# Optimization experiments

Measured on AMD Instinct MI355X. Metric: run time of the kernel, lower is better.

The kernel has to match this reference:

```python
import jax, jax.numpy as jnp
import numpy as np

N_NODES = 50000
N_EDGES = 800000
IN_FEATS = 64
OUT_FEATS = 64
EDGE_DIM = 8


def setup_inputs() -> dict:
    key = jax.random.key(0)
    k1, k2, k3, k4, k5 = jax.random.split(key, 5)
    node_feat = jax.random.normal(k1, (N_NODES, IN_FEATS), dtype=jnp.float32)
    edge_feat = jax.random.normal(k2, (N_EDGES, EDGE_DIM), dtype=jnp.float32)
    W = jax.random.normal(k3, (OUT_FEATS, IN_FEATS), dtype=jnp.float32) * (1.0 / np.sqrt(IN_FEATS))
    b = jnp.zeros((OUT_FEATS,), dtype=jnp.float32)
    src = jax.random.randint(k4, (N_EDGES,), 0, N_NODES, dtype=jnp.int64 if jax.config.jax_enable_x64 else jnp.int32)
    dst = jax.random.randint(k5, (N_EDGES,), 0, N_NODES, dtype=jnp.int64 if jax.config.jax_enable_x64 else jnp.int32)
    return {"node_feat": node_feat, "edge_feat": edge_feat, "W": W, "b": b,
            "src": src, "dst": dst}


def reference(node_feat, edge_feat, W, b, src, dst):
    # EfConv forward with aggregate='sum', node_feat.shape[1] == in_feats.
    n_nodes = node_feat.shape[0]
    edge_dim = edge_feat.shape[1]
    h_src = node_feat[src]  # [E, in_feats] gather once, reused for every slice
    aggs = []
    for k in range(edge_dim):  # small fixed loop over edge feature slices
        m = h_src * edge_feat[:, k:k + 1]                      # u_mul_e: [E, in_feats]
        aggs.append(jax.ops.segment_sum(m, dst, num_segments=n_nodes))
    agg = jnp.stack(aggs, axis=1)                              # [N, edge_dim, in_feats]
    # per-slice shared linear, then concat along feature dim
    out = jnp.einsum('nki,oi->nko', agg, W) + b                # [N, edge_dim, out_feats]
    return out.reshape(n_nodes, edge_dim * W.shape[0])         # [N, edge_dim*out_feats]
```

## Files before the change

kernel.cpp:

```cpp
#include <hip/hip_runtime.h>


#define FEATS 64
#define EDGE_DIM 8

typedef _Float16 half8 __attribute__((ext_vector_type(8)));

__global__ void __launch_bounds__(256) transform_kernel(
    const float* __restrict__ nf, const float* __restrict__ W,
    _Float16* __restrict__ t, int* __restrict__ deg, int n_nodes)
{
    __shared__ float sWt[FEATS * 65];
    __shared__ float srow[4][FEATS];
    const int tid = threadIdx.x;

    int gid = blockIdx.x * 256 + tid;
    if (gid < n_nodes) deg[gid] = 0;

    #pragma unroll
    for (int base = 0; base < FEATS * FEATS; base += 256) {
        int idx = base + tid;
        int o = idx >> 6;
        int i = idx & 63;
        sWt[i * 65 + o] = W[idx];
    }

    const int r = tid >> 6;
    const int o = tid & 63;
    const int node = blockIdx.x * 4 + r;
    if (node < n_nodes) srow[r][o] = nf[(long)node * FEATS + o];
    __syncthreads();

    if (node >= n_nodes) return;
    float sum = 0.f;
    #pragma unroll
    for (int i = 0; i < FEATS; i++)
        sum += srow[r][i] * sWt[i * 65 + o];
    t[(long)node * FEATS + o] = (_Float16)sum;
}

__global__ void __launch_bounds__(256) hist_kernel(
    const int* __restrict__ dst, int* __restrict__ deg,
    int* __restrict__ rank, int n_edges)
{
    int i4 = (blockIdx.x * 256 + threadIdx.x) * 4;
    if (i4 + 3 < n_edges) {
        int4 d = *(const int4*)(dst + i4);
        int4 r;
        r.x = atomicAdd(&deg[d.x], 1);
        r.y = atomicAdd(&deg[d.y], 1);
        r.z = atomicAdd(&deg[d.z], 1);
        r.w = atomicAdd(&deg[d.w], 1);
        *(int4*)(rank + i4) = r;
    } else {
        for (int e = i4; e < n_edges; ++e)
            rank[e] = atomicAdd(&deg[dst[e]], 1);
    }
}

__global__ void __launch_bounds__(256) partials_kernel(
    const int* __restrict__ deg, int* __restrict__ partials, int n)
{
    __shared__ int s[256];
    int i = blockIdx.x * 256 + threadIdx.x;
    s[threadIdx.x] = (i < n) ? deg[i] : 0;
    __syncthreads();
    for (int off = 128; off > 0; off >>= 1) {
        if (threadIdx.x < off) s[threadIdx.x] += s[threadIdx.x + off];
        __syncthreads();
    }
    if (threadIdx.x == 0) partials[blockIdx.x] = s[0];
}

__global__ void __launch_bounds__(256) scan_partials_kernel(
    const int* __restrict__ partials, int* __restrict__ pscan, int nb)
{
    __shared__ int s[256];
    int tid = threadIdx.x;
    s[tid] = (tid < nb) ? partials[tid] : 0;
    for (int off = 1; off < 256; off <<= 1) {
        __syncthreads();
        int x = (tid >= off) ? s[tid - off] : 0;
        __syncthreads();
        s[tid] += x;
    }
    __syncthreads();
    pscan[tid] = (tid == 0) ? 0 : s[tid - 1];
}

__global__ void __launch_bounds__(256) scan_addback_kernel(
    const int* __restrict__ deg, const int* __restrict__ pscan,
    int* __restrict__ offsets, int n, int n_edges)
{
    __shared__ int s[256];
    int tid = threadIdx.x;
    int i = blockIdx.x * 256 + tid;
    int v = (i < n) ? deg[i] : 0;
    s[tid] = v;
    for (int off = 1; off < 256; off <<= 1) {
        __syncthreads();
        int x = (tid >= off) ? s[tid - off] : 0;
        __syncthreads();
        s[tid] += x;
    }
    __syncthreads();
    if (i < n)
        offsets[i] = pscan[blockIdx.x] + s[tid] - v;
    if (blockIdx.x == 0 && tid == 0) offsets[n] = n_edges;
}

__global__ void __launch_bounds__(256) permute_ef_kernel(
    const int* __restrict__ src, const int* __restrict__ dst,
    const int* __restrict__ rank, const int* __restrict__ offsets,
    const float* __restrict__ ef,
    int* __restrict__ srcs, half8* __restrict__ efs, int n_edges)
{
    int i4 = (blockIdx.x * 256 + threadIdx.x) * 4;
    if (i4 + 3 < n_edges) {
        int4 s = *(const int4*)(src + i4);
        int4 d = *(const int4*)(dst + i4);
        int4 r = *(const int4*)(rank + i4);
        const float4* q = (const float4*)(ef + (long)i4 * EDGE_DIM);
        int p0 = offsets[d.x] + r.x;
        int p1 = offsets[d.y] + r.y;
        int p2 = offsets[d.z] + r.z;
        int p3 = offsets[d.w] + r.w;
        #pragma unroll
        for (int u = 0; u < 4; u++) {
            float4 a = q[2 * u], c = q[2 * u + 1];
            half8 h;
            h[0] = (_Float16)a.x; h[1] = (_Float16)a.y;
            h[2] = (_Float16)a.z; h[3] = (_Float16)a.w;
            h[4] = (_Float16)c.x; h[5] = (_Float16)c.y;
            h[6] = (_Float16)c.z; h[7] = (_Float16)c.w;
            int p = (u == 0) ? p0 : (u == 1) ? p1 : (u == 2) ? p2 : p3;
            efs[p] = h;
        }
        srcs[p0] = s.x; srcs[p1] = s.y; srcs[p2] = s.z; srcs[p3] = s.w;
    } else {
        for (int e = i4; e < n_edges; ++e) {
            int p = offsets[dst[e]] + rank[e];
            srcs[p] = src[e];
            const float* q = ef + (long)e * EDGE_DIM;
            half8 h;
            #pragma unroll
            for (int k = 0; k < EDGE_DIM; k++) h[k] = (_Float16)q[k];
            efs[p] = h;
        }
    }
}

#define CHUNK 16

__global__ void __launch_bounds__(256) aggregate_seq_kernel(
    const _Float16* __restrict__ t, const half8* __restrict__ efs,
    const int* __restrict__ srcs, const int* __restrict__ offsets,
    const float* __restrict__ b, float* __restrict__ out, int n_nodes)
{
    const int node = __builtin_amdgcn_readfirstlane(
        (int)((blockIdx.x * 256 + threadIdx.x) >> 6));
    const int o = threadIdx.x & 63;
    if (node >= n_nodes) return;

    const int beg = offsets[node];
    const int end = offsets[node + 1];
    float acc[EDGE_DIM];
    #pragma unroll
    for (int k = 0; k < EDGE_DIM; k++) acc[k] = 0.f;

    if (end > beg) {
        const int last = end - 1;
        for (int j = beg; j < end; j += CHUNK) {
            int sidx[CHUNK];
            #pragma unroll
            for (int u = 0; u < CHUNK; u++) {
                int jj = j + u;
                sidx[u] = srcs[jj <= last ? jj : last];
            }
            float tv[CHUNK];
            #pragma unroll
            for (int u = 0; u < CHUNK; u++)
                tv[u] = (float)t[(long)sidx[u] * FEATS + o];
            #pragma unroll
            for (int u = 0; u < CHUNK; u++) {
                int jj = j + u;
                int ej = jj <= last ? jj : last;
                float tvm = (jj <= last) ? tv[u] : 0.f;
                half8 row = efs[ej];
                #pragma unroll
                for (int k = 0; k < EDGE_DIM; k++)
                    acc[k] += (float)row[k] * tvm;
            }
        }
    }

    const float bo = b[o];
    float* op = out + (long)node * (EDGE_DIM * FEATS) + o;
    #pragma unroll
    for (int k = 0; k < EDGE_DIM; k++)
        __builtin_nontemporal_store(acc[k] + bo, op + k * FEATS);
}

extern "C" void kernel_launch(void* const* d_in, const int* in_sizes, int n_in,
                              void* d_out, int out_size, void* d_ws, size_t ws_size,
                              hipStream_t stream) {
    const float* node_feat = (const float*)d_in[0];
    const float* edge_feat = (const float*)d_in[1];
    const float* W         = (const float*)d_in[2];
    const float* b         = (const float*)d_in[3];
    const int*   src       = (const int*)d_in[4];
    const int*   dst       = (const int*)d_in[5];
    float* out = (float*)d_out;

    const int n_nodes = in_sizes[0] / FEATS;
    const int n_edges = in_sizes[4];
    const int nb_nodes = (n_nodes + 255) / 256;
    const int nb_e4    = (n_edges + 1023) / 1024;

    int* w = (int*)d_ws;
    _Float16* t   = (_Float16*)w;
    int* deg      = w + (long)n_nodes * (FEATS / 2);
    int* offsets  = deg + n_nodes;
    int* partials = offsets + n_nodes + 1;
    int* pscan    = partials + 256;
    int* rank     = pscan + 256;
    int* srcs     = rank + n_edges;
    uintptr_t ea  = ((uintptr_t)(srcs + n_edges) + 15) & ~(uintptr_t)15;
    half8* efs    = (half8*)ea;

    transform_kernel<<<(n_nodes + 3) / 4, 256, 0, stream>>>(node_feat, W, t, deg, n_nodes);
    hist_kernel<<<nb_e4, 256, 0, stream>>>(dst, deg, rank, n_edges);
    partials_kernel<<<nb_nodes, 256, 0, stream>>>(deg, partials, n_nodes);
    scan_partials_kernel<<<1, 256, 0, stream>>>(partials, pscan, nb_nodes);
    scan_addback_kernel<<<nb_nodes, 256, 0, stream>>>(deg, pscan, offsets,
                                                      n_nodes, n_edges);
    permute_ef_kernel<<<nb_e4, 256, 0, stream>>>(src, dst, rank, offsets, edge_feat,
                                                 srcs, efs, n_edges);

    const long total_ag = (long)n_nodes * 64;
    aggregate_seq_kernel<<<(int)((total_ag + 255) / 256), 256, 0, stream>>>(
        t, efs, srcs, offsets, b, out, n_nodes);
}
```

Before: 282.4 us.

## Merge histogram with node transform and replace three-pass scan with single-workgroup scan

The degree histogram and node feature transform now run in one launch, with the first blocks doing edge atomics and the rest doing the matmul, after a separate small zero kernel. The three-kernel block scan (partials, scan partials, add-back) becomes one 1024-thread workgroup doing a serial-per-thread chunked scan with wave shuffles. This cuts the number of launches from seven to five and lets histogram and transform overlap, removing launch gaps. The trade-off is that the single-workgroup scan uses one CU and strided, uncoalesced per-thread reads of about 49 elements each.

```diff
diff --git a/kernel.cpp b/kernel.cpp
--- a/kernel.cpp
+++ b/kernel.cpp
@@ -6,16 +6,40 @@
 
 typedef _Float16 half8 __attribute__((ext_vector_type(8)));
 
-__global__ void __launch_bounds__(256) transform_kernel(
+__global__ void __launch_bounds__(256) zero_kernel(int* __restrict__ p, int n)
+{
+    int i = blockIdx.x * 256 + threadIdx.x;
+    if (i < n) p[i] = 0;
+}
+
+__global__ void __launch_bounds__(256) hist_transform_kernel(
+    const int* __restrict__ dst, int* __restrict__ deg, int* __restrict__ rank,
+    int n_edges, int nbH,
     const float* __restrict__ nf, const float* __restrict__ W,
-    _Float16* __restrict__ t, int* __restrict__ deg, int n_nodes)
-{
+    _Float16* __restrict__ t, int n_nodes)
+{
+    const int tid = threadIdx.x;
+
+    if (blockIdx.x < (unsigned)nbH) {
+        int i4 = (blockIdx.x * 256 + tid) * 4;
+        if (i4 + 3 < n_edges) {
+            int4 d = *(const int4*)(dst + i4);
+            int4 r;
+            r.x = atomicAdd(&deg[d.x], 1);
+            r.y = atomicAdd(&deg[d.y], 1);
+            r.z = atomicAdd(&deg[d.z], 1);
+            r.w = atomicAdd(&deg[d.w], 1);
+            *(int4*)(rank + i4) = r;
+        } else {
+            for (int e = i4; e < n_edges; ++e)
+                rank[e] = atomicAdd(&deg[dst[e]], 1);
+        }
+        return;
+    }
+
     __shared__ float sWt[FEATS * 65];
     __shared__ float srow[4][FEATS];
-    const int tid = threadIdx.x;
-
-    int gid = blockIdx.x * 256 + tid;
-    if (gid < n_nodes) deg[gid] = 0;
+    const int bt = blockIdx.x - nbH;
 
     #pragma unroll
     for (int base = 0; base < FEATS * FEATS; base += 256) {
@@ -27,7 +51,7 @@
 
     const int r = tid >> 6;
     const int o = tid & 63;
-    const int node = blockIdx.x * 4 + r;
+    const int node = bt * 4 + r;
     if (node < n_nodes) srow[r][o] = nf[(long)node * FEATS + o];
     __syncthreads();
 
@@ -39,74 +63,45 @@
     t[(long)node * FEATS + o] = (_Float16)sum;
 }
 
-__global__ void __launch_bounds__(256) hist_kernel(
-    const int* __restrict__ dst, int* __restrict__ deg,
-    int* __restrict__ rank, int n_edges)
-{
-    int i4 = (blockIdx.x * 256 + threadIdx.x) * 4;
-    if (i4 + 3 < n_edges) {
-        int4 d = *(const int4*)(dst + i4);
-        int4 r;
-        r.x = atomicAdd(&deg[d.x], 1);
-        r.y = atomicAdd(&deg[d.y], 1);
-        r.z = atomicAdd(&deg[d.z], 1);
-        r.w = atomicAdd(&deg[d.w], 1);
-        *(int4*)(rank + i4) = r;
-    } else {
-        for (int e = i4; e < n_edges; ++e)
-            rank[e] = atomicAdd(&deg[dst[e]], 1);
-    }
-}
-
-__global__ void __launch_bounds__(256) partials_kernel(
-    const int* __restrict__ deg, int* __restrict__ partials, int n)
-{
-    __shared__ int s[256];
-    int i = blockIdx.x * 256 + threadIdx.x;
-    s[threadIdx.x] = (i < n) ? deg[i] : 0;
+__global__ void __launch_bounds__(1024) scan1wg_kernel(
+    const int* __restrict__ deg, int* __restrict__ offsets, int n, int n_edges)
+{
+    const int tid = threadIdx.x;
+    const int T = 1024;
+    const int C = (n + T - 1) / T;
+    const int base = tid * C;
+
+    int s = 0;
+    for (int j = 0; j < C; ++j) {
+        int idx = base + j;
+        if (idx < n) s += deg[idx];
+    }
+
+    const int lane = tid & 63;
+    const int wid = tid >> 6;
+    int incl = s;
+    #pragma unroll
+    for (int off = 1; off < 64; off <<= 1) {
+        int v = __shfl_up(incl, off, 64);
+        if (lane >= off) incl += v;
+    }
+    __shared__ int wsum[16];
+    __shared__ int woff[16];
+    if (lane == 63) wsum[wid] = incl;
     __syncthreads();
-    for (int off = 128; off > 0; off >>= 1) {
-        if (threadIdx.x < off) s[threadIdx.x] += s[threadIdx.x + off];
-        __syncthreads();
-    }
-    if (threadIdx.x == 0) partials[blockIdx.x] = s[0];
-}
-
-__global__ void __launch_bounds__(256) scan_partials_kernel(
-    const int* __restrict__ partials, int* __restrict__ pscan, int nb)
-{
-    __shared__ int s[256];
-    int tid = threadIdx.x;
-    s[tid] = (tid < nb) ? partials[tid] : 0;
-    for (int off = 1; off < 256; off <<= 1) {
-        __syncthreads();
-        int x = (tid >= off) ? s[tid - off] : 0;
-        __syncthreads();
-        s[tid] += x;
+    if (tid == 0) {
+        int acc = 0;
+        #pragma unroll
+        for (int i = 0; i < 16; i++) { woff[i] = acc; acc += wsum[i]; }
     }
     __syncthreads();
-    pscan[tid] = (tid == 0) ? 0 : s[tid - 1];
-}
-
-__global__ void __launch_bounds__(256) scan_addback_kernel(
-    const int* __restrict__ deg, const int* __restrict__ pscan,
-    int* __restrict__ offsets, int n, int n_edges)
-{
-    __shared__ int s[256];
-    int tid = threadIdx.x;
-    int i = blockIdx.x * 256 + tid;
-    int v = (i < n) ? deg[i] : 0;
-    s[tid] = v;
-    for (int off = 1; off < 256; off <<= 1) {
-        __syncthreads();
-        int x = (tid >= off) ? s[tid - off] : 0;
-        __syncthreads();
-        s[tid] += x;
-    }
-    __syncthreads();
-    if (i < n)
-        offsets[i] = pscan[blockIdx.x] + s[tid] - v;
-    if (blockIdx.x == 0 && tid == 0) offsets[n] = n_edges;
+
+    int run = woff[wid] + incl - s;
+    for (int j = 0; j < C; ++j) {
+        int idx = base + j;
+        if (idx < n) { offsets[idx] = run; run += deg[idx]; }
+    }
+    if (tid == T - 1) offsets[n] = n_edges;
 }
 
 __global__ void __launch_bounds__(256) permute_ef_kernel(
@@ -215,27 +210,24 @@
     const int n_nodes = in_sizes[0] / FEATS;
     const int n_edges = in_sizes[4];
     const int nb_nodes = (n_nodes + 255) / 256;
-    const int nb_e4    = (n_edges + 1023) / 1024;
+    const int nbH = (n_edges + 1023) / 1024;
+    const int nbT = (n_nodes + 3) / 4;
 
     int* w = (int*)d_ws;
     _Float16* t   = (_Float16*)w;
     int* deg      = w + (long)n_nodes * (FEATS / 2);
     int* offsets  = deg + n_nodes;
-    int* partials = offsets + n_nodes + 1;
-    int* pscan    = partials + 256;
-    int* rank     = pscan + 256;
+    int* rank     = offsets + n_nodes + 1;
     int* srcs     = rank + n_edges;
     uintptr_t ea  = ((uintptr_t)(srcs + n_edges) + 15) & ~(uintptr_t)15;
     half8* efs    = (half8*)ea;
 
-    transform_kernel<<<(n_nodes + 3) / 4, 256, 0, stream>>>(node_feat, W, t, deg, n_nodes);
-    hist_kernel<<<nb_e4, 256, 0, stream>>>(dst, deg, rank, n_edges);
-    partials_kernel<<<nb_nodes, 256, 0, stream>>>(deg, partials, n_nodes);
-    scan_partials_kernel<<<1, 256, 0, stream>>>(partials, pscan, nb_nodes);
-    scan_addback_kernel<<<nb_nodes, 256, 0, stream>>>(deg, pscan, offsets,
-                                                      n_nodes, n_edges);
-    permute_ef_kernel<<<nb_e4, 256, 0, stream>>>(src, dst, rank, offsets, edge_feat,
-                                                 srcs, efs, n_edges);
+    zero_kernel<<<nb_nodes, 256, 0, stream>>>(deg, n_nodes);
+    hist_transform_kernel<<<nbH + nbT, 256, 0, stream>>>(
+        dst, deg, rank, n_edges, nbH, node_feat, W, t, n_nodes);
+    scan1wg_kernel<<<1, 1024, 0, stream>>>(deg, offsets, n_nodes, n_edges);
+    permute_ef_kernel<<<nbH, 256, 0, stream>>>(src, dst, rank, offsets, edge_feat,
+                                               srcs, efs, n_edges);
 
     const long total_ag = (long)n_nodes * 64;
     aggregate_seq_kernel<<<(int)((total_ag + 255) / 256), 256, 0, stream>>>(
```

New measurement: 361.3 us. +27.9%, slower.
